# Kernel tuning notes

Measured on AMD Instinct MI355X. Metric: run time of the kernel, lower is better.

The kernel has to match this reference:

```python
import jax, jax.numpy as jnp
import numpy as np

N_NODES = 100000
IN_DIM = 512
HIDDEN = 64
NUM_CLASSES = 40
N_EDGES = 3200000


def setup_inputs() -> dict:
    key = jax.random.key(0)
    k1, k2, k3, k4, k5 = jax.random.split(key, 5)
    x = jax.random.normal(k1, (N_NODES, IN_DIM), dtype=jnp.float32)
    edge_index = jax.random.randint(k2, (2, N_EDGES), 0, N_NODES, dtype=jnp.int64)
    # Glorot init like PyG GCNConv, zero bias
    s1 = (6.0 / (IN_DIM + HIDDEN)) ** 0.5
    W1 = jax.random.uniform(k3, (IN_DIM, HIDDEN), jnp.float32, -s1, s1)
    b1 = jnp.zeros((HIDDEN,), jnp.float32)
    s2 = (6.0 / (HIDDEN + NUM_CLASSES)) ** 0.5
    W2 = jax.random.uniform(k4, (HIDDEN, NUM_CLASSES), jnp.float32, -s2, s2)
    b2 = jnp.zeros((NUM_CLASSES,), jnp.float32)
    return {"x": x, "edge_index": edge_index, "W1": W1, "b1": b1, "W2": W2, "b2": b2}


def _gcn_norm(edge_index, num_nodes):
    # Add self-loops, compute symmetric normalization D^-1/2 A D^-1/2 (PyG GCNConv default).
    loop = jnp.arange(num_nodes, dtype=edge_index.dtype)
    src = jnp.concatenate([edge_index[0], loop])
    dst = jnp.concatenate([edge_index[1], loop])
    deg = jax.ops.segment_sum(jnp.ones_like(src, dtype=jnp.float32), dst, num_segments=num_nodes)
    dinv = jnp.where(deg > 0, jax.lax.rsqrt(deg), 0.0)
    norm = dinv[src] * dinv[dst]  # [E+N]
    return src, dst, norm


def _gcn_conv(x, src, dst, norm, W, b, num_nodes):
    h = x @ W                                # [N, F_out]
    msg = h[src] * norm[:, None]             # gather + scale, [E+N, F_out]
    out = jax.ops.segment_sum(msg, dst, num_segments=num_nodes)  # scatter-add
    return out + b


def reference(x, edge_index, W1, b1, W2, b2):
    n = x.shape[0]
    src, dst, norm = _gcn_norm(edge_index, n)
    h = _gcn_conv(x, src, dst, norm, W1, b1, n)
    h = jax.nn.relu(h)
    # F.dropout(training=False) is identity in eval mode
    h = _gcn_conv(h, src, dst, norm, W2, b2, n)
    return jax.nn.log_softmax(h, axis=1)
```

## Files before the change

kernel.cpp:

```cpp
#include <hip/hip_runtime.h>
#include <hip/hip_bf16.h>
#include <cmath>

#define NN 100000
#define IND 512
#define HID 64
#define NC  40
#define BWN 256
#define NBKT ((NN + BWN - 1) / BWN)
#define CAP  12288
#define NBIN_BLOCKS 200

typedef unsigned int uint32;
typedef unsigned short ushort;
using short8 = __attribute__((ext_vector_type(8))) short;
using f32x4  = __attribute__((ext_vector_type(4))) float;

__device__ inline float bf_lo(uint32 u) { return __uint_as_float(u << 16); }
__device__ inline float bf_hi(uint32 u) { return __uint_as_float(u & 0xFFFF0000u); }
__device__ inline uint32 f2bf(float f) {
    uint32 u = __float_as_uint(f);
    return (u + 0x7FFFu + ((u >> 16) & 1u)) >> 16;
}
__device__ inline uint32 pack2bf(float a, float b) { return f2bf(a) | (f2bf(b) << 16); }


__global__ __launch_bounds__(256) void wt_init_kernel(const float* __restrict__ W1,
                                                      const float* __restrict__ W2,
                                                      ushort* __restrict__ w1t,
                                                      ushort* __restrict__ w2t,
                                                      int* __restrict__ gcursor) {
    int id = blockIdx.x * blockDim.x + threadIdx.x;
    if (id < IND * HID) {
        int n = id & 63, k = id >> 6;
        w1t[(size_t)n * IND + k] = (ushort)f2bf(W1[(size_t)k * HID + n]);
    } else if (id < IND * HID + 48 * HID) {
        int id2 = id - IND * HID;
        int n = id2 >> 6, k = id2 & 63;
        w2t[id2] = (n < NC) ? (ushort)f2bf(W2[(size_t)k * NC + n]) : (ushort)0;
    }
    if (id < NBKT) gcursor[id] = id * CAP;
}


__global__ __launch_bounds__(512) void bin_kernel(const int* __restrict__ src,
                                                  const int* __restrict__ dst,
                                                  int* __restrict__ gcursor,
                                                  int* __restrict__ packed, int E) {
    __shared__ int hist[NBKT], base[NBKT], cur[NBKT];
    int b = blockIdx.x, t = threadIdx.x;
    int epb = (E + gridDim.x - 1) / gridDim.x;
    int lo = b * epb;
    int hi = lo + epb; if (hi > E) hi = E;
    for (int i = t; i < NBKT; i += 512) { hist[i] = 0; cur[i] = 0; }
    __syncthreads();
    for (int e = lo + t; e < hi; e += 512) atomicAdd(&hist[dst[e] >> 8], 1);
    __syncthreads();
    for (int i = t; i < NBKT; i += 512)
        if (hist[i]) base[i] = atomicAdd(&gcursor[i], hist[i]);
    __syncthreads();
    for (int e = lo + t; e < hi; e += 512) {
        int d = dst[e], s = src[e];
        int bk = d >> 8;
        int pos = base[bk] + atomicAdd(&cur[bk], 1);
        packed[pos] = ((d & 255) << 17) | s;
    }
}


__global__ __launch_bounds__(256) void csr_bucket_kernel(const int* __restrict__ packed,
                                                         const int* __restrict__ gcursor,
                                                         int* __restrict__ rowptr,
                                                         int* __restrict__ rowend,
                                                         int* __restrict__ colx,
                                                         float* __restrict__ dinv) {
    __shared__ int hist[BWN], pfx[BWN], cur[BWN];
    int b = blockIdx.x, t = threadIdx.x;
    int nlo = b * BWN;
    int ncnt = NN - nlo; if (ncnt > BWN) ncnt = BWN;
    int ebeg = b * CAP, eend = gcursor[b];
    hist[t] = 0;
    __syncthreads();
    for (int e = ebeg + t; e < eend; e += 256) atomicAdd(&hist[packed[e] >> 17], 1);
    __syncthreads();
    int h = hist[t];
    pfx[t] = h;
    __syncthreads();
    for (int off = 1; off < 256; off <<= 1) {
        int u = (t >= off) ? pfx[t - off] : 0;
        __syncthreads();
        pfx[t] += u;
        __syncthreads();
    }
    int excl = pfx[t] - h;
    cur[t] = excl;
    int g = nlo + t;
    if (t < ncnt) {
        rowptr[g] = ebeg + excl;
        rowend[g] = ebeg + excl + h;
        dinv[g] = rsqrtf((float)(h + 1));
    }
    __syncthreads();
    for (int e = ebeg + t; e < eend; e += 256) {
        int p = packed[e];
        int dl = p >> 17;
        int s = p & 0x1FFFF;
        int pos = ebeg + atomicAdd(&cur[dl], 1);
        colx[pos] = s;
    }
}


__global__ __launch_bounds__(256) void gemm1_mfma(const float* __restrict__ x,
                                                  const ushort* __restrict__ w1t,
                                                  const float* __restrict__ dinv,
                                                  ushort* __restrict__ hs, int M) {
    __shared__ ushort As[64 * 64];
    __shared__ ushort Bs[64 * 64];
    char* Ab = (char*)As;
    char* Bb = (char*)Bs;

    int t = threadIdx.x;
    int row0 = blockIdx.x * 64;

    int srow = t >> 2;
    int klane = t & 3;
    int grow = row0 + srow; if (grow > M - 1) grow = M - 1;
    const float* xrow = x + (size_t)grow * IND;
    const char* wrow = (const char*)(w1t + (size_t)srow * IND);
    int swrow = srow * 128;
    int swx = (srow & 7) << 4;

    int l = t & 63;
    int w = t >> 6;
    int lr = l & 15;
    int lk = (l >> 4) * 16;
    int arow_b = (w * 16 + lr) * 128;
    int aswz = ((w * 16 + lr) & 7) << 4;

    f32x4 acc[4] = {};

    float4 rx[4]; uint2 rw[4];
#pragma unroll
    for (int i = 0; i < 4; ++i) {
        rx[i] = *(const float4*)(xrow + i * 16 + klane * 4);
        rw[i] = *(const uint2*)(wrow + i * 32 + klane * 8);
    }

    for (int k0 = 0; k0 < IND; k0 += 64) {
#pragma unroll
        for (int i = 0; i < 4; ++i) {
            int kb = i * 32 + klane * 8;
            uint2 pkd;
            pkd.x = pack2bf(rx[i].x, rx[i].y);
            pkd.y = pack2bf(rx[i].z, rx[i].w);
            *(uint2*)(Ab + swrow + (kb ^ swx)) = pkd;
            *(uint2*)(Bb + swrow + (kb ^ swx)) = rw[i];
        }
        __syncthreads();

        if (k0 + 64 < IND) {
#pragma unroll
            for (int i = 0; i < 4; ++i) {
                rx[i] = *(const float4*)(xrow + k0 + 64 + i * 16 + klane * 4);
                rw[i] = *(const uint2*)(wrow + (k0 + 64) * 2 + i * 32 + klane * 8);
            }
        }

        short8 a0 = *(const short8*)(Ab + arow_b + ((0 + lk) ^ aswz));
        short8 a1 = *(const short8*)(Ab + arow_b + ((64 + lk) ^ aswz));
#pragma unroll
        for (int ns = 0; ns < 4; ++ns) {
            int brow = ns * 16 + lr;
            int bswz = (brow & 7) << 4;
            short8 b0 = *(const short8*)(Bb + brow * 128 + ((0 + lk) ^ bswz));
            short8 b1 = *(const short8*)(Bb + brow * 128 + ((64 + lk) ^ bswz));
            acc[ns] = __builtin_amdgcn_mfma_f32_16x16x32_bf16(a0, b0, acc[ns], 0, 0, 0);
            acc[ns] = __builtin_amdgcn_mfma_f32_16x16x32_bf16(a1, b1, acc[ns], 0, 0, 0);
        }
        __syncthreads();
    }

    int rbase = row0 + w * 16 + (l >> 4) * 4;
    float dv[4];
#pragma unroll
    for (int j = 0; j < 4; ++j) dv[j] = (rbase + j < M) ? dinv[rbase + j] : 0.f;
#pragma unroll
    for (int ns = 0; ns < 4; ++ns) {
        int col = ns * 16 + lr;
#pragma unroll
        for (int j = 0; j < 4; ++j) {
            int row = rbase + j;
            if (row < M) hs[(size_t)row * HID + col] = (ushort)f2bf(acc[ns][j] * dv[j]);
        }
    }
}


__global__ __launch_bounds__(256) void agg1_kernel(const uint32* __restrict__ hs,
                                                   const int* __restrict__ rowptr,
                                                   const int* __restrict__ rowend,
                                                   const int* __restrict__ colx,
                                                   const float* __restrict__ dinv,
                                                   const float* __restrict__ b1,
                                                   uint32* __restrict__ h1) {
    int node = (blockIdx.x * blockDim.x + threadIdx.x) >> 5;
    int l = threadIdx.x & 31;
    if (node >= NN) return;
    int beg = rowptr[node], end = rowend[node];
    uint32 u = hs[(size_t)node * 32 + l];
    float a0 = bf_lo(u), a1 = bf_hi(u);
    int e = beg;
    int n8 = beg + ((end - beg) & ~7);
    for (; e < n8; e += 8) {
        int c[8];
#pragma unroll
        for (int j = 0; j < 8; ++j) c[j] = __builtin_nontemporal_load(&colx[e + j]);
        uint32 uu[8];
#pragma unroll
        for (int j = 0; j < 8; ++j) uu[j] = hs[(size_t)c[j] * 32 + l];
#pragma unroll
        for (int j = 0; j < 8; ++j) { a0 += bf_lo(uu[j]); a1 += bf_hi(uu[j]); }
    }
    for (; e < end; ++e) {
        uint32 ue = hs[(size_t)__builtin_nontemporal_load(&colx[e]) * 32 + l];
        a0 += bf_lo(ue); a1 += bf_hi(ue);
    }
    float d = dinv[node];
    float2 bb = *(const float2*)(b1 + 2 * l);
    float v0 = a0 * d + bb.x;
    float v1 = a1 * d + bb.y;
    v0 = v0 > 0.f ? v0 : 0.f;
    v1 = v1 > 0.f ? v1 : 0.f;
    __builtin_nontemporal_store(pack2bf(v0, v1), &h1[(size_t)node * 32 + l]);
}


__global__ __launch_bounds__(256) void gemm2_mfma(const ushort* __restrict__ h1,
                                                  const ushort* __restrict__ w2t,
                                                  const float* __restrict__ dinv,
                                                  ushort* __restrict__ h2b, int M) {
    int t = threadIdx.x;
    int w = t >> 6, l = t & 63;
    int lr = l & 15, lh = l >> 4;
    int row0 = blockIdx.x * 64 + w * 16;
    int arow = row0 + lr; if (arow > M - 1) arow = M - 1;
    const ushort* hrow = h1 + (size_t)arow * HID;

    f32x4 acc[3] = {};
#pragma unroll
    for (int ks = 0; ks < 2; ++ks) {
        short8 a = *(const short8*)(hrow + ks * 32 + lh * 8);
#pragma unroll
        for (int ns = 0; ns < 3; ++ns) {
            short8 b = *(const short8*)(w2t + (size_t)(ns * 16 + lr) * HID + ks * 32 + lh * 8);
            acc[ns] = __builtin_amdgcn_mfma_f32_16x16x32_bf16(a, b, acc[ns], 0, 0, 0);
        }
    }

    int rbase = row0 + lh * 4;
    float dv[4];
#pragma unroll
    for (int j = 0; j < 4; ++j) dv[j] = (rbase + j < M) ? dinv[rbase + j] : 0.f;
#pragma unroll
    for (int ns = 0; ns < 3; ++ns) {
        int col = ns * 16 + lr;
        if (col < NC) {
#pragma unroll
            for (int j = 0; j < 4; ++j) {
                int row = rbase + j;
                if (row < M) h2b[(size_t)row * NC + col] = (ushort)f2bf(acc[ns][j] * dv[j]);
            }
        }
    }
}


__global__ __launch_bounds__(256) void agg2_kernel(const uint32* __restrict__ h2b,
                                                   const int* __restrict__ rowptr,
                                                   const int* __restrict__ rowend,
                                                   const int* __restrict__ colx,
                                                   const float* __restrict__ dinv,
                                                   const float* __restrict__ b2,
                                                   float* __restrict__ out) {
    int node = (blockIdx.x * blockDim.x + threadIdx.x) >> 5;
    int l = threadIdx.x & 31;
    if (node >= NN) return;
    bool act = l < 20;
    int beg = rowptr[node], end = rowend[node];
    float a0 = 0.f, a1 = 0.f;
    if (act) {
        uint32 u = h2b[(size_t)node * 20 + l];
        a0 = bf_lo(u); a1 = bf_hi(u);
    }
    int e = beg;
    int n8 = beg + ((end - beg) & ~7);
    for (; e < n8; e += 8) {
        int c[8];
#pragma unroll
        for (int j = 0; j < 8; ++j) c[j] = __builtin_nontemporal_load(&colx[e + j]);
        if (act) {
            uint32 uu[8];
#pragma unroll
            for (int j = 0; j < 8; ++j) uu[j] = h2b[(size_t)c[j] * 20 + l];
#pragma unroll
            for (int j = 0; j < 8; ++j) { a0 += bf_lo(uu[j]); a1 += bf_hi(uu[j]); }
        }
    }
    for (; e < end; ++e) {
        int c = __builtin_nontemporal_load(&colx[e]);
        if (act) {
            uint32 ue = h2b[(size_t)c * 20 + l];
            a0 += bf_lo(ue); a1 += bf_hi(ue);
        }
    }

    float d = dinv[node];
    float v0 = -INFINITY, v1 = -INFINITY;
    if (act) {
        float2 bb = *(const float2*)(b2 + 2 * l);
        v0 = a0 * d + bb.x;
        v1 = a1 * d + bb.y;
    }
    float m = fmaxf(v0, v1);
#pragma unroll
    for (int off = 16; off; off >>= 1) m = fmaxf(m, __shfl_xor(m, off));
    float s = act ? (expf(v0 - m) + expf(v1 - m)) : 0.f;
#pragma unroll
    for (int off = 16; off; off >>= 1) s += __shfl_xor(s, off);
    if (act) {
        float ls = logf(s);
        __builtin_nontemporal_store(v0 - m - ls, &out[(size_t)node * NC + 2 * l]);
        __builtin_nontemporal_store(v1 - m - ls, &out[(size_t)node * NC + 2 * l + 1]);
    }
}


extern "C" void kernel_launch(void* const* d_in, const int* in_sizes, int n_in,
                              void* d_out, int out_size, void* d_ws, size_t ws_size,
                              hipStream_t stream) {
    const float* x  = (const float*)d_in[0];
    const int* ei   = (const int*)d_in[1];
    const float* W1 = (const float*)d_in[2];
    const float* b1 = (const float*)d_in[3];
    const float* W2 = (const float*)d_in[4];
    const float* b2 = (const float*)d_in[5];
    float* out = (float*)d_out;

    const int E = in_sizes[1] / 2;
    const int* src = ei;
    const int* dst = ei + E;

    char* p = (char*)d_ws;
    size_t off = 0;
    auto carve = [&](size_t bytes) {
        void* q = p + off;
        off = (off + bytes + 255) & ~(size_t)255;
        return q;
    };
    int* gcursor  = (int*)carve((size_t)NBKT * 4);
    int* rowptr   = (int*)carve((size_t)NN * 4);
    int* rowend   = (int*)carve((size_t)NN * 4);
    float* dinv   = (float*)carve((size_t)NN * 4);
    ushort* w1t   = (ushort*)carve((size_t)IND * HID * 2);
    ushort* w2t   = (ushort*)carve((size_t)48 * HID * 2);
    ushort* hs    = (ushort*)carve((size_t)NN * HID * 2);
    uint32* h1    = (uint32*)carve((size_t)NN * 32 * 4);
    ushort* h2b   = (ushort*)carve((size_t)NN * NC * 2);
    int* colx     = (int*)carve((size_t)NBKT * CAP * 4);
    int* packed   = (int*)carve((size_t)NBKT * CAP * 4);

    wt_init_kernel<<<(IND * HID + 48 * HID + 255) / 256, 256, 0, stream>>>(W1, W2, w1t, w2t, gcursor);
    bin_kernel<<<NBIN_BLOCKS, 512, 0, stream>>>(src, dst, gcursor, packed, E);
    csr_bucket_kernel<<<NBKT, 256, 0, stream>>>(packed, gcursor, rowptr, rowend, colx, dinv);
    gemm1_mfma<<<(NN + 63) / 64, 256, 0, stream>>>(x, w1t, dinv, hs, NN);
    agg1_kernel<<<(NN * 32 + 255) / 256, 256, 0, stream>>>((const uint32*)hs, rowptr, rowend, colx, dinv, b1, h1);
    gemm2_mfma<<<(NN + 63) / 64, 256, 0, stream>>>((const ushort*)h1, w2t, dinv, h2b, NN);
    agg2_kernel<<<(NN * 32 + 255) / 256, 256, 0, stream>>>((const uint32*)h2b, rowptr, rowend, colx, dinv, b2, out);
}
```

Measured before the change: 290.1 us.

## Load GEMM1 operands directly into MFMA registers, dropping LDS staging

Measured after the change: 324.9 us. 1.12x slower.

```diff
diff --git a/kernel.cpp b/kernel.cpp
--- a/kernel.cpp
+++ b/kernel.cpp
@@ -23,6 +23,8 @@
     return (u + 0x7FFFu + ((u >> 16) & 1u)) >> 16;
 }
 __device__ inline uint32 pack2bf(float a, float b) { return f2bf(a) | (f2bf(b) << 16); }
+
+union bfpack { uint32 u[4]; short8 s; };
 
 
 __global__ __launch_bounds__(256) void wt_init_kernel(const float* __restrict__ W1,
@@ -115,73 +117,32 @@
                                                   const ushort* __restrict__ w1t,
                                                   const float* __restrict__ dinv,
                                                   ushort* __restrict__ hs, int M) {
-    __shared__ ushort As[64 * 64];
-    __shared__ ushort Bs[64 * 64];
-    char* Ab = (char*)As;
-    char* Bb = (char*)Bs;
-
     int t = threadIdx.x;
-    int row0 = blockIdx.x * 64;
-
-    int srow = t >> 2;
-    int klane = t & 3;
-    int grow = row0 + srow; if (grow > M - 1) grow = M - 1;
-    const float* xrow = x + (size_t)grow * IND;
-    const char* wrow = (const char*)(w1t + (size_t)srow * IND);
-    int swrow = srow * 128;
-    int swx = (srow & 7) << 4;
-
-    int l = t & 63;
-    int w = t >> 6;
-    int lr = l & 15;
-    int lk = (l >> 4) * 16;
-    int arow_b = (w * 16 + lr) * 128;
-    int aswz = ((w * 16 + lr) & 7) << 4;
+    int w = t >> 6, l = t & 63;
+    int lr = l & 15, lh = l >> 4;
+    int row0 = blockIdx.x * 64 + w * 16;
+    int arow = row0 + lr; if (arow > M - 1) arow = M - 1;
+    const float* xrow = x + (size_t)arow * IND;
 
     f32x4 acc[4] = {};
 
-    float4 rx[4]; uint2 rw[4];
-#pragma unroll
-    for (int i = 0; i < 4; ++i) {
-        rx[i] = *(const float4*)(xrow + i * 16 + klane * 4);
-        rw[i] = *(const uint2*)(wrow + i * 32 + klane * 8);
-    }
-
-    for (int k0 = 0; k0 < IND; k0 += 64) {
-#pragma unroll
-        for (int i = 0; i < 4; ++i) {
-            int kb = i * 32 + klane * 8;
-            uint2 pkd;
-            pkd.x = pack2bf(rx[i].x, rx[i].y);
-            pkd.y = pack2bf(rx[i].z, rx[i].w);
-            *(uint2*)(Ab + swrow + (kb ^ swx)) = pkd;
-            *(uint2*)(Bb + swrow + (kb ^ swx)) = rw[i];
-        }
-        __syncthreads();
-
-        if (k0 + 64 < IND) {
-#pragma unroll
-            for (int i = 0; i < 4; ++i) {
-                rx[i] = *(const float4*)(xrow + k0 + 64 + i * 16 + klane * 4);
-                rw[i] = *(const uint2*)(wrow + (k0 + 64) * 2 + i * 32 + klane * 8);
-            }
-        }
-
-        short8 a0 = *(const short8*)(Ab + arow_b + ((0 + lk) ^ aswz));
-        short8 a1 = *(const short8*)(Ab + arow_b + ((64 + lk) ^ aswz));
+#pragma unroll 2
+    for (int k0 = 0; k0 < IND; k0 += 32) {
+        float4 p0 = *(const float4*)(xrow + k0 + lh * 8);
+        float4 p1 = *(const float4*)(xrow + k0 + lh * 8 + 4);
+        bfpack ap;
+        ap.u[0] = pack2bf(p0.x, p0.y);
+        ap.u[1] = pack2bf(p0.z, p0.w);
+        ap.u[2] = pack2bf(p1.x, p1.y);
+        ap.u[3] = pack2bf(p1.z, p1.w);
 #pragma unroll
         for (int ns = 0; ns < 4; ++ns) {
-            int brow = ns * 16 + lr;
-            int bswz = (brow & 7) << 4;
-            short8 b0 = *(const short8*)(Bb + brow * 128 + ((0 + lk) ^ bswz));
-            short8 b1 = *(const short8*)(Bb + brow * 128 + ((64 + lk) ^ bswz));
-            acc[ns] = __builtin_amdgcn_mfma_f32_16x16x32_bf16(a0, b0, acc[ns], 0, 0, 0);
-            acc[ns] = __builtin_amdgcn_mfma_f32_16x16x32_bf16(a1, b1, acc[ns], 0, 0, 0);
-        }
-        __syncthreads();
-    }
-
-    int rbase = row0 + w * 16 + (l >> 4) * 4;
+            short8 b = *(const short8*)(w1t + (size_t)(ns * 16 + lr) * IND + k0 + lh * 8);
+            acc[ns] = __builtin_amdgcn_mfma_f32_16x16x32_bf16(ap.s, b, acc[ns], 0, 0, 0);
+        }
+    }
+
+    int rbase = row0 + lh * 4;
     float dv[4];
 #pragma unroll
     for (int j = 0; j < 4; ++j) dv[j] = (rbase + j < M) ? dinv[rbase + j] : 0.f;
```
